# Kernel optimization log

Hardware: AMD Instinct MI355X
Metric: run time of the kernel (lower is better)

Reference implementation:

```python
import jax, jax.numpy as jnp
import numpy as np

EPS = 1e-12

def _normalize(x, axis=-1):
    # matches torch F.normalize: x / max(||x||, eps)
    n = jnp.sqrt(jnp.sum(x * x, axis=axis, keepdims=True))
    return x / jnp.maximum(n, EPS)

def setup_inputs() -> dict:
    key = jax.random.key(0)
    k1, k2, k3, k4, k5 = jax.random.split(key, 5)
    B, D, N = 65536, 512, 64
    feature = jax.random.normal(k1, (B, D), dtype=jnp.float32)
    target = jax.random.randint(k2, (B, N), 0, 2, dtype=jnp.int32)
    W = jax.random.normal(k3, (N, 2, D), dtype=jnp.float32) * 0.05
    b = jax.random.normal(k4, (N, 2), dtype=jnp.float32) * 0.01
    u = jax.random.normal(k5, (N, 2), dtype=jnp.float32)
    return {"feature": feature, "target": target, "W": W, "b": b, "u": u}

def reference(feature, target, W, b, u):
    # spectral norm, one power iteration per head (torch default n_power_iterations=1)
    v = _normalize(jnp.einsum('nod,no->nd', W, u))      # [N, D]
    u1 = _normalize(jnp.einsum('nod,nd->no', W, v))      # [N, 2]
    # u, v are buffers (no grad through them in torch)
    u_s = jax.lax.stop_gradient(u1)
    v_s = jax.lax.stop_gradient(v)
    sigma = jnp.einsum('no,nod,nd->n', u_s, W, v_s)      # [N]
    W_sn = W / sigma[:, None, None]
    # dropout in eval mode = identity; fused batched matmul over all heads
    pred = jnp.einsum('bd,nod->bno', feature, W_sn) + b[None]   # [B, N, 2]
    output = jnp.argmax(pred, axis=2)                           # [B, N]
    # CrossEntropyLoss with soft targets: class dim is dim=1 (nclass), as in torch code
    onehot = jax.nn.one_hot(target, 2, dtype=jnp.float32)       # [B, N, 2]
    logp = jax.nn.log_softmax(pred, axis=1)                     # softmax over nclass dim
    loss = jnp.mean(-jnp.sum(onehot * logp, axis=1))            # mean over B and the 2-dim
    return pred, output, loss
```

## Files before the change

kernel.cpp:

```cpp
#include <hip/hip_runtime.h>
#include <math.h>

typedef __bf16 bf16x8 __attribute__((ext_vector_type(8)));
typedef float  f32x4  __attribute__((ext_vector_type(4)));

#define BROWS 65536
#define DIM   512
#define NHEAD 64
#define NCOL  128

#define PRED_SZ  ((size_t)BROWS * NCOL)
#define ARG_BASE PRED_SZ
#define LOSS_IDX (PRED_SZ + (size_t)BROWS * NHEAD)
#define BF_OFF   ARG_BASE
#define PART_OFF (ARG_BASE + 1056 * (size_t)NHEAD)
#define FIX_ROWS 1088


__global__ __launch_bounds__(64) void spectral_kernel(
    const float* __restrict__ W, const float* __restrict__ u,
    __bf16* __restrict__ Bfrag)
{
    int n = blockIdx.x;
    int lane = threadIdx.x;

    const float* W0 = W + (size_t)n * 2 * DIM;
    const float* W1 = W0 + DIM;
    float u0 = u[2 * n], u1v = u[2 * n + 1];

    float w0[8], w1[8], vr[8];
    {
        float4 a0 = *(const float4*)(W0 + lane * 8);
        float4 a1 = *(const float4*)(W0 + lane * 8 + 4);
        float4 b0 = *(const float4*)(W1 + lane * 8);
        float4 b1 = *(const float4*)(W1 + lane * 8 + 4);
        w0[0]=a0.x; w0[1]=a0.y; w0[2]=a0.z; w0[3]=a0.w;
        w0[4]=a1.x; w0[5]=a1.y; w0[6]=a1.z; w0[7]=a1.w;
        w1[0]=b0.x; w1[1]=b0.y; w1[2]=b0.z; w1[3]=b0.w;
        w1[4]=b1.x; w1[5]=b1.y; w1[6]=b1.z; w1[7]=b1.w;
    }

    float ss = 0.f;
#pragma unroll
    for (int j = 0; j < 8; ++j) {
        vr[j] = fmaf(w0[j], u0, w1[j] * u1v);
        ss = fmaf(vr[j], vr[j], ss);
    }
#pragma unroll
    for (int m = 32; m >= 1; m >>= 1) ss += __shfl_xor(ss, m, 64);
    float inv_n = 1.f / fmaxf(sqrtf(ss), 1e-12f);

    float s0 = 0.f, s1 = 0.f;
#pragma unroll
    for (int j = 0; j < 8; ++j) {
        float v = vr[j] * inv_n;
        s0 = fmaf(w0[j], v, s0);
        s1 = fmaf(w1[j], v, s1);
    }
#pragma unroll
    for (int m = 32; m >= 1; m >>= 1) {
        s0 += __shfl_xor(s0, m, 64);
        s1 += __shfl_xor(s1, m, 64);
    }
    float nu = sqrtf(fmaf(s0, s0, s1 * s1));
    float inv_nu = 1.f / fmaxf(nu, 1e-12f);
    float sigma = fmaf(s0 * inv_nu, s0, (s1 * inv_nu) * s1);
    float inv_sigma = 1.f / sigma;

    int kc = lane >> 3;
    int s  = (lane >> 2) & 1;
    int q  = lane & 3;
#pragma unroll
    for (int o = 0; o < 2; ++o) {
        int col = 2 * n + o;
        int nt = col >> 4, cc = col & 15;
        bf16x8 hi, lo;
#pragma unroll
        for (int j = 0; j < 8; ++j) {
            float x = (o ? w1[j] : w0[j]) * inv_sigma;
            __bf16 h = (__bf16)x;
            hi[j] = h;
            lo[j] = (__bf16)(x - (float)h);
        }
        size_t base = (size_t)kc * 16384 + (size_t)(q * 16 + cc) * 8;
        *(bf16x8*)(Bfrag + base + (size_t)((0 * 8 + nt) * 2 + s) * 512) = hi;
        *(bf16x8*)(Bfrag + base + (size_t)((1 * 8 + nt) * 2 + s) * 512) = lo;
    }
}

#define CVT8(H, L, F0, F1) {                                   \
    float _v; __bf16 _h;                                       \
    _v = (F0).x; _h = (__bf16)_v; H[0] = _h; L[0] = (__bf16)(_v - (float)_h); \
    _v = (F0).y; _h = (__bf16)_v; H[1] = _h; L[1] = (__bf16)(_v - (float)_h); \
    _v = (F0).z; _h = (__bf16)_v; H[2] = _h; L[2] = (__bf16)(_v - (float)_h); \
    _v = (F0).w; _h = (__bf16)_v; H[3] = _h; L[3] = (__bf16)(_v - (float)_h); \
    _v = (F1).x; _h = (__bf16)_v; H[4] = _h; L[4] = (__bf16)(_v - (float)_h); \
    _v = (F1).y; _h = (__bf16)_v; H[5] = _h; L[5] = (__bf16)(_v - (float)_h); \
    _v = (F1).z; _h = (__bf16)_v; H[6] = _h; L[6] = (__bf16)(_v - (float)_h); \
    _v = (F1).w; _h = (__bf16)_v; H[7] = _h; L[7] = (__bf16)(_v - (float)_h); }

__device__ __forceinline__ void gld_lds16(const __bf16* g, __bf16* l) {
    __builtin_amdgcn_global_load_lds(
        (const __attribute__((address_space(1))) void*)g,
        (__attribute__((address_space(3))) void*)l, 16, 0, 0);
}

__global__ __launch_bounds__(256, 4) void gemm_fused(
    const float* __restrict__ A, const int* __restrict__ target,
    const __bf16* __restrict__ Bfrag, const float* __restrict__ bias,
    float* __restrict__ pred, float* __restrict__ outArg,
    float* __restrict__ partials)
{
    __shared__ __bf16 Bs[16384];
    __shared__ float wsum[4];

    int tid  = threadIdx.x;
    int wave = tid >> 6;
    int lane = tid & 63;
    int q = lane >> 4;
    int c = lane & 15;
    int rowBase = blockIdx.x * 64 + wave * 16;

    f32x4 acc[8] = {};

    const float*  ap = A + (size_t)(rowBase + c) * DIM + q * 8;
    const __bf16* gB = Bfrag + (size_t)(wave * 8) * 512 + lane * 8;
    __bf16*       lB = Bs + (size_t)(wave * 8) * 512;

    float4 xa = *(const float4*)(ap + 0);
    float4 xb = *(const float4*)(ap + 4);
    float4 ya = *(const float4*)(ap + 32);
    float4 yb = *(const float4*)(ap + 36);

    for (int kc = 0; kc < 8; ++kc) {
#pragma unroll
        for (int t = 0; t < 8; ++t)
            gld_lds16(gB + (size_t)kc * 16384 + t * 512, lB + t * 512);

        int nb = (kc < 7) ? (kc + 1) * 64 : 0;
        float4 nxa = *(const float4*)(ap + nb);
        float4 nxb = *(const float4*)(ap + nb + 4);
        float4 nya = *(const float4*)(ap + nb + 32);
        float4 nyb = *(const float4*)(ap + nb + 36);

        __syncthreads();

        bf16x8 ah, al;
        CVT8(ah, al, xa, xb);
#pragma unroll
        for (int nt = 0; nt < 8; ++nt) {
            bf16x8 bh = *(const bf16x8*)(Bs + (size_t)((nt * 2 + 0) * 512) + lane * 8);
            bf16x8 bl = *(const bf16x8*)(Bs + (size_t)(((8 + nt) * 2 + 0) * 512) + lane * 8);
            acc[nt] = __builtin_amdgcn_mfma_f32_16x16x32_bf16(ah, bh, acc[nt], 0, 0, 0);
            acc[nt] = __builtin_amdgcn_mfma_f32_16x16x32_bf16(al, bh, acc[nt], 0, 0, 0);
            acc[nt] = __builtin_amdgcn_mfma_f32_16x16x32_bf16(ah, bl, acc[nt], 0, 0, 0);
        }
        CVT8(ah, al, ya, yb);
#pragma unroll
        for (int nt = 0; nt < 8; ++nt) {
            bf16x8 bh = *(const bf16x8*)(Bs + (size_t)((nt * 2 + 1) * 512) + lane * 8);
            bf16x8 bl = *(const bf16x8*)(Bs + (size_t)(((8 + nt) * 2 + 1) * 512) + lane * 8);
            acc[nt] = __builtin_amdgcn_mfma_f32_16x16x32_bf16(ah, bh, acc[nt], 0, 0, 0);
            acc[nt] = __builtin_amdgcn_mfma_f32_16x16x32_bf16(al, bh, acc[nt], 0, 0, 0);
            acc[nt] = __builtin_amdgcn_mfma_f32_16x16x32_bf16(ah, bl, acc[nt], 0, 0, 0);
        }
        __syncthreads();

        xa = nxa; xb = nxb; ya = nya; yb = nyb;
    }

    float bv[8];
#pragma unroll
    for (int nt = 0; nt < 8; ++nt) bv[nt] = bias[nt * 16 + c];

    float lp = 0.f;
    bool doA = (rowBase >= FIX_ROWS);
#pragma unroll
    for (int reg = 0; reg < 4; ++reg) {
        int row = rowBase + q * 4 + reg;
        float p[8];
#pragma unroll
        for (int nt = 0; nt < 8; ++nt) p[nt] = acc[nt][reg] + bv[nt];
#pragma unroll
        for (int nt = 0; nt < 8; ++nt)
            pred[(size_t)row * NCOL + nt * 16 + c] = p[nt];

        float M = p[0];
#pragma unroll
        for (int nt = 1; nt < 8; ++nt) M = fmaxf(M, p[nt]);
        M = fmaxf(M, __shfl_xor(M, 2, 64));
        M = fmaxf(M, __shfl_xor(M, 4, 64));
        M = fmaxf(M, __shfl_xor(M, 8, 64));
        float Mx = __shfl_xor(M, 1, 64);

        float sE = 0.f;
#pragma unroll
        for (int nt = 0; nt < 8; ++nt) sE += expf(p[nt] - M);
        sE += __shfl_xor(sE, 2, 64);
        sE += __shfl_xor(sE, 4, 64);
        sE += __shfl_xor(sE, 8, 64);
        float sX = __shfl_xor(sE, 1, 64);

        float Lown = M + logf(sE);
        float Loth = Mx + logf(sX);
        float L0 = (c & 1) ? Loth : Lown;
        float L1 = (c & 1) ? Lown : Loth;

        float pn[8];
#pragma unroll
        for (int nt = 0; nt < 8; ++nt) pn[nt] = __shfl_xor(p[nt], 1, 64);

        if ((c & 1) == 0) {
            const int* trow = target + (size_t)row * NHEAD;
            float* arow = outArg + (size_t)row * NHEAD;
#pragma unroll
            for (int nt = 0; nt < 8; ++nt) {
                int head = nt * 8 + (c >> 1);
                int t = trow[head];
                lp += t ? (L1 - pn[nt]) : (L0 - p[nt]);
                if (doA) arow[head] = (pn[nt] > p[nt]) ? 1.f : 0.f;
            }
        }
    }

#pragma unroll
    for (int m = 32; m >= 1; m >>= 1) lp += __shfl_xor(lp, m, 64);
    if (lane == 0) wsum[wave] = lp;
    __syncthreads();
    if (tid == 0)
        partials[blockIdx.x] = (wsum[0] + wsum[1]) + (wsum[2] + wsum[3]);
}

__global__ __launch_bounds__(256) void fixup_kernel(
    const float* __restrict__ pred, const float* __restrict__ partials,
    float* __restrict__ outArg, float* __restrict__ lossOut)
{
    int tid = threadIdx.x;
    if (blockIdx.x == 0) {
        __shared__ double red[256];
        double s = 0.0;
#pragma unroll
        for (int i = 0; i < 4; ++i) s += (double)partials[tid * 4 + i];
        red[tid] = s;
        __syncthreads();
        for (int m = 128; m >= 1; m >>= 1) {
            if (tid < m) red[tid] += red[tid + m];
            __syncthreads();
        }
        if (tid == 0) lossOut[0] = (float)(red[0] / 131072.0);
        __syncthreads();
        int row = 1056 + (tid >> 3);
        int hb = (tid & 7) * 8;
        const float* pr = pred + (size_t)row * NCOL;
        float* ar = outArg + (size_t)row * NHEAD;
#pragma unroll
        for (int h = 0; h < 8; ++h) {
            float a = pr[2 * (hb + h)], b = pr[2 * (hb + h) + 1];
            ar[hb + h] = (b > a) ? 1.f : 0.f;
        }
    } else {
        int row = (blockIdx.x - 1) * 16 + (tid >> 4);
        int hb = (tid & 15) * 4;
        const float* pr = pred + (size_t)row * NCOL;
        float* ar = outArg + (size_t)row * NHEAD;
#pragma unroll
        for (int h = 0; h < 4; ++h) {
            float a = pr[2 * (hb + h)], b = pr[2 * (hb + h) + 1];
            ar[hb + h] = (b > a) ? 1.f : 0.f;
        }
    }
}

extern "C" void kernel_launch(void* const* d_in, const int* in_sizes, int n_in,
                              void* d_out, int out_size, void* d_ws, size_t ws_size,
                              hipStream_t stream) {
    const float* feature = (const float*)d_in[0];
    const int*   target  = (const int*)d_in[1];
    const float* W       = (const float*)d_in[2];
    const float* bias    = (const float*)d_in[3];
    const float* u       = (const float*)d_in[4];

    float* out     = (float*)d_out;
    float* pred    = out;
    float* outArg  = out + ARG_BASE;
    float* lossOut = out + LOSS_IDX;
    __bf16* Bfrag  = (__bf16*)(out + BF_OFF);
    float* partial = out + PART_OFF;

    spectral_kernel<<<NHEAD, 64, 0, stream>>>(W, u, Bfrag);
    gemm_fused<<<BROWS / 64, 256, 0, stream>>>(feature, target, Bfrag, bias,
                                               pred, outArg, partial);
    fixup_kernel<<<67, 256, 0, stream>>>(pred, partial, outArg, lossOut);
}
```

Measured before the change: 242.4 us.

## Drop split-bf16 compensation and use 1024-thread blocks with half-K LDS staging

The GEMM stops splitting both operands into hi and lo bf16 parts and keeps a single bf16 product, so each tile needs one MFMA instead of three and half the B fragment data. Blocks grow to 1024 threads (16 waves, 256 rows) and stage B in LDS in two halves of K, which cuts the number of block-wide barriers and how often B is reloaded. The cost is lower precision for pred, which may change argmax ties and the loss beyond tolerance. The larger block may also reduce occupancy, and the loss partials shrink to 256 entries.

```diff
diff --git a/kernel.cpp b/kernel.cpp
--- a/kernel.cpp
+++ b/kernel.cpp
@@ -67,37 +67,25 @@
     float sigma = fmaf(s0 * inv_nu, s0, (s1 * inv_nu) * s1);
     float inv_sigma = 1.f / sigma;
 
-    int kc = lane >> 3;
-    int s  = (lane >> 2) & 1;
-    int q  = lane & 3;
+    int kc2 = lane >> 2;
+    int q   = lane & 3;
 #pragma unroll
     for (int o = 0; o < 2; ++o) {
         int col = 2 * n + o;
         int nt = col >> 4, cc = col & 15;
-        bf16x8 hi, lo;
-#pragma unroll
-        for (int j = 0; j < 8; ++j) {
-            float x = (o ? w1[j] : w0[j]) * inv_sigma;
-            __bf16 h = (__bf16)x;
-            hi[j] = h;
-            lo[j] = (__bf16)(x - (float)h);
-        }
-        size_t base = (size_t)kc * 16384 + (size_t)(q * 16 + cc) * 8;
-        *(bf16x8*)(Bfrag + base + (size_t)((0 * 8 + nt) * 2 + s) * 512) = hi;
-        *(bf16x8*)(Bfrag + base + (size_t)((1 * 8 + nt) * 2 + s) * 512) = lo;
-    }
-}
-
-#define CVT8(H, L, F0, F1) {                                   \
-    float _v; __bf16 _h;                                       \
-    _v = (F0).x; _h = (__bf16)_v; H[0] = _h; L[0] = (__bf16)(_v - (float)_h); \
-    _v = (F0).y; _h = (__bf16)_v; H[1] = _h; L[1] = (__bf16)(_v - (float)_h); \
-    _v = (F0).z; _h = (__bf16)_v; H[2] = _h; L[2] = (__bf16)(_v - (float)_h); \
-    _v = (F0).w; _h = (__bf16)_v; H[3] = _h; L[3] = (__bf16)(_v - (float)_h); \
-    _v = (F1).x; _h = (__bf16)_v; H[4] = _h; L[4] = (__bf16)(_v - (float)_h); \
-    _v = (F1).y; _h = (__bf16)_v; H[5] = _h; L[5] = (__bf16)(_v - (float)_h); \
-    _v = (F1).z; _h = (__bf16)_v; H[6] = _h; L[6] = (__bf16)(_v - (float)_h); \
-    _v = (F1).w; _h = (__bf16)_v; H[7] = _h; L[7] = (__bf16)(_v - (float)_h); }
+        bf16x8 hi;
+#pragma unroll
+        for (int j = 0; j < 8; ++j)
+            hi[j] = (__bf16)((o ? w1[j] : w0[j]) * inv_sigma);
+        *(bf16x8*)(Bfrag + (size_t)(kc2 * 8 + nt) * 512 + (q * 16 + cc) * 8) = hi;
+    }
+}
+
+#define CVT8H(H, F0, F1) {            \
+    H[0] = (__bf16)(F0).x; H[1] = (__bf16)(F0).y; \
+    H[2] = (__bf16)(F0).z; H[3] = (__bf16)(F0).w; \
+    H[4] = (__bf16)(F1).x; H[5] = (__bf16)(F1).y; \
+    H[6] = (__bf16)(F1).z; H[7] = (__bf16)(F1).w; }
 
 __device__ __forceinline__ void gld_lds16(const __bf16* g, __bf16* l) {
     __builtin_amdgcn_global_load_lds(
@@ -105,68 +93,57 @@
         (__attribute__((address_space(3))) void*)l, 16, 0, 0);
 }
 
-__global__ __launch_bounds__(256, 4) void gemm_fused(
+__global__ __launch_bounds__(1024, 4) void gemm_fused(
     const float* __restrict__ A, const int* __restrict__ target,
     const __bf16* __restrict__ Bfrag, const float* __restrict__ bias,
     float* __restrict__ pred, float* __restrict__ outArg,
     float* __restrict__ partials)
 {
-    __shared__ __bf16 Bs[16384];
-    __shared__ float wsum[4];
+    __shared__ __bf16 Bs[32768];
 
     int tid  = threadIdx.x;
     int wave = tid >> 6;
     int lane = tid & 63;
     int q = lane >> 4;
     int c = lane & 15;
-    int rowBase = blockIdx.x * 64 + wave * 16;
+    int rowBase = blockIdx.x * 256 + wave * 16;
 
     f32x4 acc[8] = {};
 
-    const float*  ap = A + (size_t)(rowBase + c) * DIM + q * 8;
-    const __bf16* gB = Bfrag + (size_t)(wave * 8) * 512 + lane * 8;
-    __bf16*       lB = Bs + (size_t)(wave * 8) * 512;
-
-    float4 xa = *(const float4*)(ap + 0);
-    float4 xb = *(const float4*)(ap + 4);
-    float4 ya = *(const float4*)(ap + 32);
-    float4 yb = *(const float4*)(ap + 36);
-
-    for (int kc = 0; kc < 8; ++kc) {
-#pragma unroll
-        for (int t = 0; t < 8; ++t)
-            gld_lds16(gB + (size_t)kc * 16384 + t * 512, lB + t * 512);
-
-        int nb = (kc < 7) ? (kc + 1) * 64 : 0;
-        float4 nxa = *(const float4*)(ap + nb);
-        float4 nxb = *(const float4*)(ap + nb + 4);
-        float4 nya = *(const float4*)(ap + nb + 32);
-        float4 nyb = *(const float4*)(ap + nb + 36);
-
+    const float* ap = A + (size_t)(rowBase + c) * DIM + q * 8;
+    float4 x0 = *(const float4*)(ap);
+    float4 x1 = *(const float4*)(ap + 4);
+
+#pragma unroll
+    for (int half = 0; half < 2; ++half) {
+        if (half) __syncthreads();
+        {
+            const __bf16* gB = Bfrag + (size_t)half * 32768
+                             + (size_t)(wave * 4) * 512 + lane * 8;
+            __bf16* lB = Bs + (size_t)(wave * 4) * 512;
+#pragma unroll
+            for (int t = 0; t < 4; ++t)
+                gld_lds16(gB + t * 512, lB + t * 512);
+        }
         __syncthreads();
 
-        bf16x8 ah, al;
-        CVT8(ah, al, xa, xb);
-#pragma unroll
-        for (int nt = 0; nt < 8; ++nt) {
-            bf16x8 bh = *(const bf16x8*)(Bs + (size_t)((nt * 2 + 0) * 512) + lane * 8);
-            bf16x8 bl = *(const bf16x8*)(Bs + (size_t)(((8 + nt) * 2 + 0) * 512) + lane * 8);
-            acc[nt] = __builtin_amdgcn_mfma_f32_16x16x32_bf16(ah, bh, acc[nt], 0, 0, 0);
-            acc[nt] = __builtin_amdgcn_mfma_f32_16x16x32_bf16(al, bh, acc[nt], 0, 0, 0);
-            acc[nt] = __builtin_amdgcn_mfma_f32_16x16x32_bf16(ah, bl, acc[nt], 0, 0, 0);
-        }
-        CVT8(ah, al, ya, yb);
-#pragma unroll
-        for (int nt = 0; nt < 8; ++nt) {
-            bf16x8 bh = *(const bf16x8*)(Bs + (size_t)((nt * 2 + 1) * 512) + lane * 8);
-            bf16x8 bl = *(const bf16x8*)(Bs + (size_t)(((8 + nt) * 2 + 1) * 512) + lane * 8);
-            acc[nt] = __builtin_amdgcn_mfma_f32_16x16x32_bf16(ah, bh, acc[nt], 0, 0, 0);
-            acc[nt] = __builtin_amdgcn_mfma_f32_16x16x32_bf16(al, bh, acc[nt], 0, 0, 0);
-            acc[nt] = __builtin_amdgcn_mfma_f32_16x16x32_bf16(ah, bl, acc[nt], 0, 0, 0);
-        }
-        __syncthreads();
-
-        xa = nxa; xb = nxb; ya = nya; yb = nyb;
+#pragma unroll
+        for (int kc = 0; kc < 8; ++kc) {
+            float4 n0, n1;
+            if (!(half == 1 && kc == 7)) {
+                int kn = half * 256 + kc * 32 + 32;
+                n0 = *(const float4*)(ap + kn);
+                n1 = *(const float4*)(ap + kn + 4);
+            }
+            bf16x8 ah;
+            CVT8H(ah, x0, x1);
+#pragma unroll
+            for (int nt = 0; nt < 8; ++nt) {
+                bf16x8 b = *(const bf16x8*)(Bs + (size_t)(kc * 8 + nt) * 512 + lane * 8);
+                acc[nt] = __builtin_amdgcn_mfma_f32_16x16x32_bf16(ah, b, acc[nt], 0, 0, 0);
+            }
+            if (!(half == 1 && kc == 7)) { x0 = n0; x1 = n1; }
+        }
     }
 
     float bv[8];
@@ -225,10 +202,16 @@
 
 #pragma unroll
     for (int m = 32; m >= 1; m >>= 1) lp += __shfl_xor(lp, m, 64);
+    float* wsum = (float*)Bs;
+    __syncthreads();
     if (lane == 0) wsum[wave] = lp;
     __syncthreads();
-    if (tid == 0)
-        partials[blockIdx.x] = (wsum[0] + wsum[1]) + (wsum[2] + wsum[3]);
+    if (tid == 0) {
+        float s = 0.f;
+#pragma unroll
+        for (int w = 0; w < 16; ++w) s += wsum[w];
+        partials[blockIdx.x] = s;
+    }
 }
 
 __global__ __launch_bounds__(256) void fixup_kernel(
@@ -238,10 +221,7 @@
     int tid = threadIdx.x;
     if (blockIdx.x == 0) {
         __shared__ double red[256];
-        double s = 0.0;
-#pragma unroll
-        for (int i = 0; i < 4; ++i) s += (double)partials[tid * 4 + i];
-        red[tid] = s;
+        red[tid] = (double)partials[tid];
         __syncthreads();
         for (int m = 128; m >= 1; m >>= 1) {
             if (tid < m) red[tid] += red[tid + m];
@@ -288,7 +268,7 @@
     float* partial = out + PART_OFF;
 
     spectral_kernel<<<NHEAD, 64, 0, stream>>>(W, u, Bfrag);
-    gemm_fused<<<BROWS / 64, 256, 0, stream>>>(feature, target, Bfrag, bias,
-                                               pred, outArg, partial);
+    gemm_fused<<<BROWS / 256, 1024, 0, stream>>>(feature, target, Bfrag, bias,
+                                                 pred, outArg, partial);
     fixup_kernel<<<67, 256, 0, stream>>>(pred, partial, outArg, lossOut);
 }
```

After: 243.5 us. Within noise of the previous version (+0.5%).
